# Optimization experiments

Measured on AMD Instinct MI355X. Metric: run time of the kernel, lower is better.

The kernel has to match this reference:

```python
import jax, jax.numpy as jnp
import numpy as np

B, T, D, H, S, C = 4, 2048, 1024, 16, 64, 64
LN_EPS = 1e-5
GN_EPS = 1e-5


def _layernorm(x, g, b):
    m = x.mean(-1, keepdims=True)
    v = ((x - m) ** 2).mean(-1, keepdims=True)
    return (x - m) * jax.lax.rsqrt(v + LN_EPS) * g + b


def _act_quant_ste(x):
    # clip_val computed on detached activations (matches x.detach() in torch)
    clip_val = jnp.clip(jnp.abs(jax.lax.stop_gradient(x)).mean(-1, keepdims=True), 1e-8) * 2.5
    scale = clip_val / 127.0
    xs = x / scale
    xc = jnp.clip(xs, -127.0, 127.0)
    xq = jax.lax.stop_gradient(jnp.round(xc) - xs) + xs  # straight-through round
    return xq * scale


def _weight_quant_ste(w):
    scale = jnp.clip(jnp.abs(jax.lax.stop_gradient(w)).mean(), 1e-8)
    wn = w / scale
    wc = jnp.clip(wn, -1.0, 1.0)
    wq = jax.lax.stop_gradient(jnp.round(wc) - wn) + wn  # ternary STE
    return wq * scale


def _bitlinear(x, w, g, b):
    xq = _act_quant_ste(_layernorm(x, g, b))
    wq = _weight_quant_ste(w)
    return xq @ wq.T


def _wkv_train(r, k, v, log_decay, u):
    # r,k,v: (B,H,T,S). Chunked WKV recurrence, chunk size C, state (B,H,S,S).
    dt = r.dtype
    w = jnp.exp(-jnp.exp(log_decay))            # (H,S)
    u_exp = jnp.exp(u)                          # (H,S)
    log_w = jnp.log(jnp.clip(w, 1e-38))
    t = jnp.arange(C, dtype=dt)
    # faithful to torch: diff[a,b] = clamp(t[b]-t[a],0), mask[a,b] = (t[b] >= t[a])
    diff = jnp.clip(t[None, :] - t[:, None], 0.0)
    mask = (t[None, :] >= t[:, None]).astype(dt)
    M = mask[:, :, None, None] * jnp.exp(diff[:, :, None, None] * log_w[None, None])  # (C,C,H,S)
    decay_cross = jnp.transpose(jnp.exp((t + 1.0)[:, None, None] * log_w[None]), (1, 0, 2))  # (H,C,S)
    decay_to_end = jnp.exp((C - 1.0 - t)[:, None, None] * log_w[None])  # (C,H,S)
    w_C = jnp.exp(C * log_w)  # (H,S)

    def chunk(state, rkv):
        r_c, k_c, v_c = rkv                                      # (B,H,C,S)
        kv = k_c[..., :, None] * v_c[..., None, :]               # (B,H,C,S,S)
        A = jnp.einsum('tihs,bhiso->bhtso', M, kv)               # intra-chunk
        A = A + decay_cross[None, :, :, :, None] * state[:, :, None, :, :]  # cross-chunk
        A = A + u_exp[None, :, None, :, None] * kv               # bonus term
        y_c = jnp.einsum('bhts,bhtso->bhto', r_c, A)             # (B,H,C,S)
        new_state = w_C[None, :, :, None] * state + jnp.einsum('chs,bhcso->bhso', decay_to_end, kv)
        return new_state, y_c

    chunk = jax.checkpoint(chunk)  # mirrors torch gradient checkpointing per chunk
    nC = T // C
    resh = lambda a: jnp.transpose(a.reshape(B, H, nC, C, S), (2, 0, 1, 3, 4))
    state0 = jnp.zeros((B, H, S, S), dt)
    _, ys = jax.lax.scan(chunk, state0, (resh(r), resh(k), resh(v)))  # ys: (nC,B,H,C,S)
    return jnp.transpose(ys, (1, 2, 0, 3, 4)).reshape(B, H, T, S)


def reference(x, mu_r, mu_k, mu_v, mu_g, log_decay, u, proj_w, ln_g, ln_b, gn_g, gn_b):
    # token shift: previous token, zero-padded at t=0
    xs = jnp.pad(x, ((0, 0), (1, 0), (0, 0)))[:, :-1]
    xx = xs - x

    def proj(inp, i):
        return _bitlinear(inp, proj_w[i], ln_g[i], ln_b[i])

    to_heads = lambda a: jnp.transpose(a.reshape(B, T, H, S), (0, 2, 1, 3))
    r = to_heads(proj(x + xx * mu_r, 0))
    k = to_heads(proj(x + xx * mu_k, 1))
    v = to_heads(proj(x + xx * mu_v, 2))
    g = proj(x + xx * mu_g, 3)

    y = _wkv_train(r, k, v, log_decay, u)                        # (B,H,T,S)
    y = jnp.transpose(y, (0, 2, 1, 3)).reshape(B, T, D)

    # GroupNorm(H groups over D) applied per (b,t) position
    yg = y.reshape(B, T, H, S)
    m = yg.mean(-1, keepdims=True)
    va = ((yg - m) ** 2).mean(-1, keepdims=True)
    yn = ((yg - m) * jax.lax.rsqrt(va + GN_EPS)).reshape(B, T, D)
    y = yn * gn_g + gn_b

    y = y * jax.nn.silu(g)
    return proj(y, 4)


def setup_inputs() -> dict:
    key = jax.random.key(0)
    ks = jax.random.split(key, 8)
    lid, n_layer = 16, 32
    base_decay = -4.0 + 3.0 * (lid / (n_layer - 1))
    ld = base_decay + 2.0 * (jnp.arange(S, dtype=jnp.float32) / max(S - 1, 1))
    log_decay = jnp.broadcast_to(ld, (H, S)).astype(jnp.float32)
    mu = lambda k: jax.random.uniform(k, (1, 1, D), jnp.float32, -1e-4, 1e-4)
    return {
        'x': jax.random.normal(ks[0], (B, T, D), jnp.float32),
        'mu_r': mu(ks[1]),
        'mu_k': mu(ks[2]),
        'mu_v': mu(ks[3]),
        'mu_g': mu(ks[4]),
        'log_decay': log_decay,
        'u': jax.random.normal(ks[5], (H, S), jnp.float32) * 0.02,
        'proj_w': jax.random.normal(ks[6], (5, D, D), jnp.float32) * 0.02,
        'ln_g': jnp.ones((5, D), jnp.float32),
        'ln_b': jnp.zeros((5, D), jnp.float32),
        'gn_g': jnp.ones((D,), jnp.float32),
        'gn_b': jnp.zeros((D,), jnp.float32),
    }
```

## Files before the change

### kernel.cpp

```cpp
#include <hip/hip_runtime.h>
#include <hip/hip_bf16.h>

#define BB 4
#define TT 2048
#define DD 1024
#define HH 16
#define SS 64
#define CH 64
#define NC (TT/CH)
#define M_ROWS (BB*TT)
#define COL 68

typedef __hip_bfloat16 bf16;
using int4v  = __attribute__((ext_vector_type(4))) int;
using short8 = __attribute__((ext_vector_type(8))) short;
using f32x4  = __attribute__((ext_vector_type(4))) float;

#if defined(__has_builtin)
#if __has_builtin(__builtin_amdgcn_global_load_lds)
#define HAVE_GLL 1
#endif
#if __has_builtin(__builtin_amdgcn_mfma_i32_16x16x64_i8)
#define HAVE_I8K64 1
#endif
#endif

#ifdef HAVE_GLL
static __device__ __forceinline__ void gload16(const void* g, void* l) {
  __builtin_amdgcn_global_load_lds(
      (const __attribute__((address_space(1))) void*)g,
      (__attribute__((address_space(3))) void*)l, 16, 0, 0);
}
#endif

static __device__ __forceinline__ float wave_sum(float v) {
  #pragma unroll
  for (int d = 1; d < 64; d <<= 1) v += __shfl_xor(v, d);
  return v;
}

static __device__ __forceinline__ float block_sum4(float v, float* slot, int tid) {
  float w = wave_sum(v);
  if ((tid & 63) == 0) slot[tid >> 6] = w;
  __syncthreads();
  return slot[0] + slot[1] + slot[2] + slot[3];
}

static __device__ __forceinline__ int pack4(int a, int b, int c, int d) {
  return (a & 0xff) | ((b & 0xff) << 8) | ((c & 0xff) << 16) | ((d & 0xff) << 24);
}

static __device__ __forceinline__ unsigned packsplit(float f) {
  unsigned b  = __float_as_uint(f);
  unsigned hb = b & 0xffff0000u;
  float fl = f - __uint_as_float(hb);
  unsigned lb = __float_as_uint(fl) >> 16;
  return hb | lb;
}

static __device__ __forceinline__ void unpk8(const unsigned* q, short8& h, short8& l) {
  uint4 q0 = *(const uint4*)q;
  uint4 q1 = *(const uint4*)(q + 4);
  unsigned ar[8] = {q0.x, q0.y, q0.z, q0.w, q1.x, q1.y, q1.z, q1.w};
  #pragma unroll
  for (int e = 0; e < 8; e++) {
    h[e] = (short)(ar[e] >> 16);
    l[e] = (short)(ar[e] & 0xffffu);
  }
}

__global__ __launch_bounds__(64) void k_tab(const float* __restrict__ log_decay,
                                            const float* __restrict__ u,
                                            float* __restrict__ P1t,
                                            float* __restrict__ P2t,
                                            float* __restrict__ K1Ft,
                                            float* __restrict__ K2Ft,
                                            float* __restrict__ EUt) {
  int blk = blockIdx.x;
  int h = blk >> 6, t = blk & 63;
  int s = threadIdx.x;
  float d = expf(log_decay[h * SS + s]);
  size_t idx = (size_t)blk * SS + s;
  P1t[idx]  = expf(d * (float)t);
  P2t[idx]  = expf(-d * (float)(t + 1));
  K1Ft[idx] = expf(-d * (float)t);
  K2Ft[idx] = expf(-d * (float)(63 - t));
  if (t == 0) EUt[h * SS + s] = expf(u[h * SS + s]);
}

__global__ __launch_bounds__(256) void k_wscale_part(const float* __restrict__ w,
                                                     double* __restrict__ wpart) {
  __shared__ double red[256];
  int i = blockIdx.x, b = blockIdx.y, tid = threadIdx.x;
  const float* base = w + (size_t)i * DD * DD + (size_t)b * 16384;
  double s = 0.0;
  #pragma unroll
  for (int j = 0; j < 64; j++) s += (double)fabsf(base[tid + j * 256]);
  red[tid] = s; __syncthreads();
  for (int o = 128; o > 0; o >>= 1) {
    if (tid < o) red[tid] += red[tid + o];
    __syncthreads();
  }
  if (tid == 0) wpart[i * 64 + b] = red[0];
}

__global__ __launch_bounds__(64) void k_wscale_fin(const double* __restrict__ wpart,
                                                   float* __restrict__ wscale) {
  int i = blockIdx.x;
  if (threadIdx.x == 0) {
    double s = 0.0;
    for (int b = 0; b < 64; b++) s += wpart[i * 64 + b];
    wscale[i] = fmaxf((float)(s * (1.0 / (DD * DD))), 1e-8f);
  }
}

__global__ __launch_bounds__(256) void k_wquant(const float* __restrict__ w,
                                                const float* __restrict__ wscale,
                                                char* __restrict__ wq) {
  int idx4 = (blockIdx.x * 256 + threadIdx.x) * 4;
  int i = idx4 >> 20;
  float ws = wscale[i];
  float4 w4 = *(const float4*)&w[idx4];
  float vals[4] = {w4.x, w4.y, w4.z, w4.w};
  int q[4];
  #pragma unroll
  for (int j = 0; j < 4; j++) {
    float wn = fminf(fmaxf(vals[j] / ws, -1.f), 1.f);
    q[j] = (int)rintf(wn);
  }
  *(int*)&wq[idx4] = pack4(q[0], q[1], q[2], q[3]);
}

__global__ __launch_bounds__(256) void k_prep_quant(
    const float* __restrict__ x, const float* __restrict__ mu_r,
    const float* __restrict__ mu_k, const float* __restrict__ mu_v,
    const float* __restrict__ mu_g, const float* __restrict__ ln_g,
    const float* __restrict__ ln_b, char* __restrict__ xq,
    float* __restrict__ ascale) {
  __shared__ float slots[12 * 4];
  int m = blockIdx.x, tid = threadIdx.x;
  int t = m & (TT - 1);
  const float* xr = x + (size_t)m * DD;
  int d4 = tid * 4;
  float4 xv4 = *(const float4*)&xr[d4];
  float4 xs4 = (t > 0) ? *(const float4*)&xr[d4 - DD]
                       : (float4){0.f, 0.f, 0.f, 0.f};
  float xv[4] = {xv4.x, xv4.y, xv4.z, xv4.w};
  float xs[4] = {xs4.x, xs4.y, xs4.z, xs4.w};
  const float* mus[4] = {mu_r, mu_k, mu_v, mu_g};
  #pragma unroll 1
  for (int i = 0; i < 4; i++) {
    float4 mu4 = *(const float4*)&mus[i][d4];
    float mu[4] = {mu4.x, mu4.y, mu4.z, mu4.w};
    float inp[4];
    #pragma unroll
    for (int j = 0; j < 4; j++) inp[j] = xv[j] + (xs[j] - xv[j]) * mu[j];
    float mean = block_sum4(inp[0] + inp[1] + inp[2] + inp[3],
                            &slots[(i * 3 + 0) * 4], tid) * (1.f / DD);
    float var = 0.f;
    #pragma unroll
    for (int j = 0; j < 4; j++) { float dv = inp[j] - mean; var += dv * dv; }
    var = block_sum4(var, &slots[(i * 3 + 1) * 4], tid) * (1.f / DD);
    float rstd = 1.f / sqrtf(var + 1e-5f);
    float4 lg4 = *(const float4*)&ln_g[i * DD + d4];
    float4 lb4 = *(const float4*)&ln_b[i * DD + d4];
    float lg[4] = {lg4.x, lg4.y, lg4.z, lg4.w};
    float lb[4] = {lb4.x, lb4.y, lb4.z, lb4.w};
    float ln[4]; float aabs = 0.f;
    #pragma unroll
    for (int j = 0; j < 4; j++) {
      ln[j] = (inp[j] - mean) * rstd * lg[j] + lb[j];
      aabs += fabsf(ln[j]);
    }
    float meanabs = block_sum4(aabs, &slots[(i * 3 + 2) * 4], tid) * (1.f / DD);
    float scale = fmaxf(meanabs, 1e-8f) * 2.5f * (1.f / 127.f);
    int q[4];
    #pragma unroll
    for (int j = 0; j < 4; j++)
      q[j] = (int)rintf(fminf(fmaxf(ln[j] / scale, -127.f), 127.f));
    *(int*)&xq[((size_t)i * M_ROWS + m) * DD + d4] = pack4(q[0], q[1], q[2], q[3]);
    if (tid == 0) ascale[i * M_ROWS + m] = scale;
  }
}

__global__ __launch_bounds__(512) void k_gemm(
    const char* __restrict__ Axq, const char* __restrict__ Wq,
    const float* __restrict__ ascale, const float* __restrict__ wscale,
    int projbase, float* __restrict__ outF) {
  __shared__ __align__(16) char As[3][256 * 64];
  __shared__ __align__(16) char Bs[3][256 * 64];
  int tid = threadIdx.x;
  int wvid = tid >> 6, lane = tid & 63;
  int wm = wvid >> 2, wn = wvid & 3;
  int m0 = blockIdx.x * 256, n0 = blockIdx.y * 256;
  int z = blockIdx.z;
  int proj = projbase + z;
  const char* Ap = Axq + ((size_t)z * M_ROWS + m0) * DD;
  const char* Wp = Wq + ((size_t)proj * DD + n0) * DD;
  int4v acc[8][4];
  #pragma unroll
  for (int i = 0; i < 8; i++)
    #pragma unroll
    for (int j = 0; j < 4; j++) acc[i][j] = (int4v){0, 0, 0, 0};

  int frow = lane & 15, fslot = lane >> 4;
  int srow_lo = tid >> 2;
  int sslot0  = tid & 3;

  auto stage_pass = [&](int k0, int q, char* Ad, char* Bd) {
    int rr = ((q & 1) << 7) + srow_lo;
    int sl = sslot0 ^ ((rr >> 1) & 3);
    if (q < 2) {
#ifdef HAVE_GLL
      gload16(&Ap[(size_t)rr * DD + k0 + sl * 16], &Ad[(q & 1) * 8192 + tid * 16]);
#else
      *(uint4*)&Ad[(q & 1) * 8192 + tid * 16] =
          *(const uint4*)&Ap[(size_t)rr * DD + k0 + sl * 16];
#endif
    } else {
#ifdef HAVE_GLL
      gload16(&Wp[(size_t)rr * DD + k0 + sl * 16], &Bd[(q & 1) * 8192 + tid * 16]);
#else
      *(uint4*)&Bd[(q & 1) * 8192 + tid * 16] =
          *(const uint4*)&Wp[(size_t)rr * DD + k0 + sl * 16];
#endif
    }
  };

  #pragma unroll
  for (int q = 0; q < 4; q++) stage_pass(0, q, As[0], Bs[0]);
  #pragma unroll
  for (int q = 0; q < 4; q++) stage_pass(64, q, As[1], Bs[1]);
#ifdef HAVE_GLL
  asm volatile("s_waitcnt vmcnt(4)" ::: "memory");
  __builtin_amdgcn_s_barrier();
#else
  __syncthreads();
#endif

  for (int kt = 0; kt < 16; ++kt) {
    const char* Abuf = As[kt % 3];
    const char* Bbuf = Bs[kt % 3];
    char* Anx = As[(kt + 2) % 3];
    char* Bnx = Bs[(kt + 2) % 3];
    int k0n = (kt + 2) * 64;
    bool do_stage = (kt + 2) < 16;
    int4v bfr[4];
    #pragma unroll
    for (int j = 0; j < 4; j++) {
      int r = 64 * wn + 16 * j + frow;
      bfr[j] = *(const int4v*)&Bbuf[r * 64 + (fslot ^ ((r >> 1) & 3)) * 16];
    }
    #pragma unroll
    for (int p = 0; p < 4; p++) {
      if (do_stage) stage_pass(k0n, p, Anx, Bnx);
      int4v af[2];
      #pragma unroll
      for (int e = 0; e < 2; e++) {
        int r = 128 * wm + 16 * (2 * p + e) + frow;
        af[e] = *(const int4v*)&Abuf[r * 64 + (fslot ^ ((r >> 1) & 3)) * 16];
      }
      __builtin_amdgcn_s_setprio(1);
#ifdef HAVE_I8K64
      #pragma unroll
      for (int e = 0; e < 2; e++)
        #pragma unroll
        for (int j = 0; j < 4; j++)
          acc[2 * p + e][j] =
              __builtin_amdgcn_mfma_i32_16x16x64_i8(af[e], bfr[j], acc[2 * p + e][j], 0, 0, 0);
#else
      #pragma unroll
      for (int e = 0; e < 2; e++)
        #pragma unroll
        for (int j = 0; j < 4; j++)
          #pragma unroll
          for (int hh2 = 0; hh2 < 2; hh2++) {
            long a8, b8;
            memcpy(&a8, ((const char*)&af[e]) + hh2 * 8, 8);
            memcpy(&b8, ((const char*)&bfr[j]) + hh2 * 8, 8);
            acc[2 * p + e][j] =
                __builtin_amdgcn_mfma_i32_16x16x32_i8(a8, b8, acc[2 * p + e][j], 0, 0, 0);
          }
#endif
      __builtin_amdgcn_s_setprio(0);
    }
    if (kt < 15) {
#ifdef HAVE_GLL
      if (kt + 2 < 16) asm volatile("s_waitcnt vmcnt(4)" ::: "memory");
      else             asm volatile("s_waitcnt vmcnt(0)" ::: "memory");
      __builtin_amdgcn_s_barrier();
#else
      __syncthreads();
#endif
    }
  }

  const float* asc = ascale + (size_t)z * M_ROWS + m0;
  float wsc = wscale[proj];
  int col = lane & 15, rg = lane >> 4;
  #pragma unroll
  for (int i = 0; i < 8; i++) {
    #pragma unroll
    for (int r = 0; r < 4; r++) {
      int mm = 128 * wm + 16 * i + rg * 4 + r;
      float s = asc[mm] * wsc;
      #pragma unroll
      for (int j = 0; j < 4; j++) {
        int nn = 64 * wn + 16 * j + col;
        outF[((size_t)z * M_ROWS + m0 + mm) * DD + (n0 + nn)] = (float)acc[i][j][r] * s;
      }
    }
  }
}

__global__ __launch_bounds__(256) void k_inj_mm(const float* __restrict__ rkvg,
                                                const float* __restrict__ K2Ft,
                                                float* __restrict__ states) {
#if defined(__HIP_DEVICE_COMPILE__)
  __shared__ __align__(16) unsigned k2t[64 * COL];
  __shared__ __align__(16) unsigned vtsh[64 * COL];
  int blk = blockIdx.x, tid = threadIdx.x;
  int n = blk & (NC - 1), h = (blk >> 5) & (HH - 1), b = blk >> 9;
  size_t rowbase = ((size_t)b * TT + n * CH) * DD + h * SS;
  const float* Kp = rkvg + (size_t)1 * M_ROWS * DD + rowbase;
  const float* Vp = rkvg + (size_t)2 * M_ROWS * DD + rowbase;
  const float* K2h = K2Ft + (size_t)h * SS * SS;

  int s_me = tid & 63, c0 = tid >> 6;
  #pragma unroll 4
  for (int j = 0; j < 16; j++) {
    int c = c0 + 4 * j;
    float kv = Kp[(size_t)c * DD + s_me];
    float vv = Vp[(size_t)c * DD + s_me];
    k2t[s_me * COL + c] = packsplit(kv * K2h[(size_t)c * SS + s_me]);
    vtsh[s_me * COL + c] = packsplit(vv);
  }
  __syncthreads();

  int wid = tid >> 6, lane = tid & 63;
  int s_row = wid * 16 + (lane & 15);
  int koff = (lane >> 4) * 8;
  short8 ah[2], al[2];
  #pragma unroll
  for (int kh = 0; kh < 2; kh++)
    unpk8(&k2t[s_row * COL + kh * 32 + koff], ah[kh], al[kh]);

  float* st = states + (size_t)blk * SS * SS;
  #pragma unroll 1
  for (int ot = 0; ot < 4; ot++) {
    int o_row = ot * 16 + (lane & 15);
    f32x4 acc = {0.f, 0.f, 0.f, 0.f};
    #pragma unroll
    for (int kh = 0; kh < 2; kh++) {
      short8 vh, vl;
      unpk8(&vtsh[o_row * COL + kh * 32 + koff], vh, vl);
      acc = __builtin_amdgcn_mfma_f32_16x16x32_bf16(ah[kh], vh, acc, 0, 0, 0);
      acc = __builtin_amdgcn_mfma_f32_16x16x32_bf16(ah[kh], vl, acc, 0, 0, 0);
      acc = __builtin_amdgcn_mfma_f32_16x16x32_bf16(al[kh], vh, acc, 0, 0, 0);
    }
    #pragma unroll
    for (int rr = 0; rr < 4; rr++) {
      int s = wid * 16 + (lane >> 4) * 4 + rr;
      int o = ot * 16 + (lane & 15);
      st[(size_t)s * SS + o] = acc[rr];
    }
  }
#endif
}

__global__ __launch_bounds__(256) void k_scan(const float* __restrict__ log_decay,
                                              float* __restrict__ states) {
  int blk = blockIdx.x;
  int bh = blk >> 4, sb = blk & 15;
  int h = bh & (HH - 1);
  int tid = threadIdx.x;
  int js = tid >> 6, o = tid & 63;
  int s = sb * 4 + js;
  float wC = expf(-64.f * expf(log_decay[h * SS + s]));
  float* base = states + (size_t)bh * NC * SS * SS + (size_t)s * SS + o;
  float inj[NC];
  #pragma unroll
  for (int n = 0; n < NC; n++) inj[n] = base[(size_t)n * SS * SS];
  float cur = 0.f;
  #pragma unroll
  for (int n = 0; n < NC; n++) {
    base[(size_t)n * SS * SS] = cur;
    cur = fmaf(wC, cur, inj[n]);
  }
}

__global__ __launch_bounds__(256) void k_wkv_mm(const float* __restrict__ rkvg,
                                                const float* __restrict__ states,
                                                const float* __restrict__ P1t,
                                                const float* __restrict__ P2t,
                                                const float* __restrict__ K1Ft,
                                                const float* __restrict__ EUt,
                                                float* __restrict__ Y) {
#if defined(__HIP_DEVICE_COMPILE__)
  __shared__ __align__(16) float    rsh[64 * COL];
  __shared__ __align__(16) unsigned k1sh[64 * COL];
  __shared__ __align__(16) unsigned vtsh[64 * COL];
  unsigned* Pls = (unsigned*)rsh;

  int blk = blockIdx.x, tid = threadIdx.x;
  int n = blk & (NC - 1), h = (blk >> 5) & (HH - 1), b = blk >> 9;
  size_t rowbase = ((size_t)b * TT + n * CH) * DD + h * SS;
  const float* Rp = rkvg + rowbase;
  const float* Kp = rkvg + (size_t)1 * M_ROWS * DD + rowbase;
  const float* Vp = rkvg + (size_t)2 * M_ROWS * DD + rowbase;
  const float* stp = states + (size_t)blk * SS * SS;
  const float* P1h = P1t + (size_t)h * SS * SS;
  const float* P2h = P2t + (size_t)h * SS * SS;
  const float* K1h = K1Ft + (size_t)h * SS * SS;

  int s_me = tid & 63, c0 = tid >> 6;
  float stv[16];
  #pragma unroll 4
  for (int j = 0; j < 16; j++) {
    int c = c0 + 4 * j;
    float rv = Rp[(size_t)c * DD + s_me];
    float kv = Kp[(size_t)c * DD + s_me];
    float vv = Vp[(size_t)c * DD + s_me];
    stv[j] = stp[(size_t)c * SS + s_me];
    rsh[c * COL + s_me] = rv;
    k1sh[c * COL + s_me] = packsplit(kv * K1h[(size_t)c * SS + s_me]);
    vtsh[s_me * COL + c] = packsplit(vv);
  }
  __syncthreads();

  int wid = tid >> 6, lane = tid & 63;
  int t_row = wid * 16 + (lane & 15);
  int koff = (lane >> 4) * 8;

  short8 a1h[2], a1l[2], a2h[2], a2l[2];
  #pragma unroll
  for (int kh = 0; kh < 2; kh++) {
    int sb0 = kh * 32 + koff;
    size_t tb = (size_t)t_row * SS + sb0;
    float4 p1a = *(const float4*)&P1h[tb], p1b = *(const float4*)&P1h[tb + 4];
    float4 p2a = *(const float4*)&P2h[tb], p2b = *(const float4*)&P2h[tb + 4];
    float4 rva = *(const float4*)&rsh[t_row * COL + sb0];
    float4 rvb = *(const float4*)&rsh[t_row * COL + sb0 + 4];
    float p1[8] = {p1a.x, p1a.y, p1a.z, p1a.w, p1b.x, p1b.y, p1b.z, p1b.w};
    float p2[8] = {p2a.x, p2a.y, p2a.z, p2a.w, p2b.x, p2b.y, p2b.z, p2b.w};
    float rv[8] = {rva.x, rva.y, rva.z, rva.w, rvb.x, rvb.y, rvb.z, rvb.w};
    #pragma unroll
    for (int e = 0; e < 8; e++) {
      unsigned u1 = packsplit(rv[e] * p1[e]);
      unsigned u2 = packsplit(rv[e] * p2[e]);
      a1h[kh][e] = (short)(u1 >> 16); a1l[kh][e] = (short)(u1 & 0xffffu);
      a2h[kh][e] = (short)(u2 >> 16); a2l[kh][e] = (short)(u2 & 0xffffu);
    }
  }

  #pragma unroll 1
  for (int it = 0; it < 4; it++) {
    int i_row = it * 16 + (lane & 15);
    f32x4 acc = {0.f, 0.f, 0.f, 0.f};
    f32x4 accu = {0.f, 0.f, 0.f, 0.f};
    bool anyKeep = (it >= wid);
    bool diag = (it == wid);
    if (anyKeep) {
      #pragma unroll
      for (int kh = 0; kh < 2; kh++) {
        const unsigned* q = &k1sh[i_row * COL + kh * 32 + koff];
        uint4 q0 = *(const uint4*)q;
        uint4 q1 = *(const uint4*)(q + 4);
        unsigned ar[8] = {q0.x, q0.y, q0.z, q0.w, q1.x, q1.y, q1.z, q1.w};
        short8 bh, bl;
        #pragma unroll
        for (int e = 0; e < 8; e++) {
          bh[e] = (short)(ar[e] >> 16);
          bl[e] = (short)(ar[e] & 0xffffu);
        }
        acc = __builtin_amdgcn_mfma_f32_16x16x32_bf16(a1h[kh], bh, acc, 0, 0, 0);
        acc = __builtin_amdgcn_mfma_f32_16x16x32_bf16(a1h[kh], bl, acc, 0, 0, 0);
        acc = __builtin_amdgcn_mfma_f32_16x16x32_bf16(a1l[kh], bh, acc, 0, 0, 0);
        if (diag) {
          int sb0 = kh * 32 + koff;
          float4 eua = *(const float4*)&EUt[h * SS + sb0];
          float4 eub = *(const float4*)&EUt[h * SS + sb0 + 4];
          float eu[8] = {eua.x, eua.y, eua.z, eua.w, eub.x, eub.y, eub.z, eub.w};
          short8 bhu, blu;
          #pragma unroll
          for (int e = 0; e < 8; e++) {
            float k1f = __uint_as_float(ar[e] & 0xffff0000u)
                      + __uint_as_float((ar[e] & 0xffffu) << 16);
            unsigned pu = packsplit(k1f * eu[e]);
            bhu[e] = (short)(pu >> 16); blu[e] = (short)(pu & 0xffffu);
          }
          accu = __builtin_amdgcn_mfma_f32_16x16x32_bf16(a1h[kh], bhu, accu, 0, 0, 0);
          accu = __builtin_amdgcn_mfma_f32_16x16x32_bf16(a1h[kh], blu, accu, 0, 0, 0);
          accu = __builtin_amdgcn_mfma_f32_16x16x32_bf16(a1l[kh], bhu, accu, 0, 0, 0);
        }
      }
    }
    #pragma unroll
    for (int rr = 0; rr < 4; rr++) {
      int trow = wid * 16 + (lane >> 4) * 4 + rr;
      int icol = it * 16 + (lane & 15);
      float p = acc[rr];
      p = (icol < trow) ? 0.f : p;
      if (icol == trow) p += accu[rr];
      Pls[trow * COL + icol] = packsplit(p);
    }
  }
  __syncthreads();

  unsigned* stsh = k1sh;
  #pragma unroll
  for (int j = 0; j < 16; j++) {
    int c = c0 + 4 * j;
    stsh[s_me * COL + c] = packsplit(stv[j]);
  }
  __syncthreads();

  float* Yb = Y + ((size_t)b * TT + n * CH) * DD + h * SS;
  #pragma unroll 1
  for (int ot = 0; ot < 4; ot++) {
    int o_row = ot * 16 + (lane & 15);
    f32x4 acc = {0.f, 0.f, 0.f, 0.f};
    #pragma unroll
    for (int kh = 0; kh < 2; kh++) {
      short8 ph, pl, vh, vl, sh2, sl2;
      unpk8(&Pls[t_row * COL + kh * 32 + koff], ph, pl);
      unpk8(&vtsh[o_row * COL + kh * 32 + koff], vh, vl);
      acc = __builtin_amdgcn_mfma_f32_16x16x32_bf16(ph, vh, acc, 0, 0, 0);
      acc = __builtin_amdgcn_mfma_f32_16x16x32_bf16(ph, vl, acc, 0, 0, 0);
      acc = __builtin_amdgcn_mfma_f32_16x16x32_bf16(pl, vh, acc, 0, 0, 0);
      unpk8(&stsh[o_row * COL + kh * 32 + koff], sh2, sl2);
      acc = __builtin_amdgcn_mfma_f32_16x16x32_bf16(a2h[kh], sh2, acc, 0, 0, 0);
      acc = __builtin_amdgcn_mfma_f32_16x16x32_bf16(a2h[kh], sl2, acc, 0, 0, 0);
      acc = __builtin_amdgcn_mfma_f32_16x16x32_bf16(a2l[kh], sh2, acc, 0, 0, 0);
    }
    #pragma unroll
    for (int rr = 0; rr < 4; rr++) {
      int trow = wid * 16 + (lane >> 4) * 4 + rr;
      int oc = ot * 16 + (lane & 15);
      Yb[(size_t)trow * DD + oc] = acc[rr];
    }
  }
#endif
}

__global__ __launch_bounds__(256) void k_post(const float* __restrict__ Y,
                                              const float* __restrict__ G,
                                              const float* __restrict__ gn_g,
                                              const float* __restrict__ gn_b,
                                              const float* __restrict__ lg,
                                              const float* __restrict__ lb,
                                              char* __restrict__ xq4,
                                              float* __restrict__ ascale4) {
  __shared__ float slots[3 * 4];
  __shared__ float gmean[HH], grstd[HH];
  int m = blockIdx.x, tid = threadIdx.x;
  int d4 = tid * 4;
  float4 y4v = *(const float4*)&Y[(size_t)m * DD + d4];
  float4 g4v = *(const float4*)&G[(size_t)m * DD + d4];
  float y4[4] = {y4v.x, y4v.y, y4v.z, y4v.w};
  float g4[4] = {g4v.x, g4v.y, g4v.z, g4v.w};
  {
    float s = y4[0] + y4[1] + y4[2] + y4[3];
    s += __shfl_xor(s, 1); s += __shfl_xor(s, 2);
    s += __shfl_xor(s, 4); s += __shfl_xor(s, 8);
    float mn = s * (1.f / SS);
    float v2 = 0.f;
    #pragma unroll
    for (int q = 0; q < 4; q++) { float dv = y4[q] - mn; v2 += dv * dv; }
    v2 += __shfl_xor(v2, 1); v2 += __shfl_xor(v2, 2);
    v2 += __shfl_xor(v2, 4); v2 += __shfl_xor(v2, 8);
    if ((tid & 15) == 0) {
      gmean[tid >> 4] = mn;
      grstd[tid >> 4] = 1.f / sqrtf(v2 * (1.f / SS) + 1e-5f);
    }
  }
  __syncthreads();
  int hh = tid >> 4;
  float4 gg4 = *(const float4*)&gn_g[d4];
  float4 gb4 = *(const float4*)&gn_b[d4];
  float gg[4] = {gg4.x, gg4.y, gg4.z, gg4.w};
  float gb[4] = {gb4.x, gb4.y, gb4.z, gb4.w};
  float z[4];
  #pragma unroll
  for (int j = 0; j < 4; j++) {
    float yn = (y4[j] - gmean[hh]) * grstd[hh] * gg[j] + gb[j];
    float gv = g4[j];
    z[j] = yn * (gv / (1.f + expf(-gv)));
  }
  float mean = block_sum4(z[0] + z[1] + z[2] + z[3], &slots[0], tid) * (1.f / DD);
  float var = 0.f;
  #pragma unroll
  for (int j = 0; j < 4; j++) { float dv = z[j] - mean; var += dv * dv; }
  var = block_sum4(var, &slots[4], tid) * (1.f / DD);
  float rstd = 1.f / sqrtf(var + 1e-5f);
  float4 lg4 = *(const float4*)&lg[d4];
  float4 lb4 = *(const float4*)&lb[d4];
  float lgv[4] = {lg4.x, lg4.y, lg4.z, lg4.w};
  float lbv[4] = {lb4.x, lb4.y, lb4.z, lb4.w};
  float ln[4]; float aabs = 0.f;
  #pragma unroll
  for (int j = 0; j < 4; j++) {
    ln[j] = (z[j] - mean) * rstd * lgv[j] + lbv[j];
    aabs += fabsf(ln[j]);
  }
  float meanabs = block_sum4(aabs, &slots[8], tid) * (1.f / DD);
  float scale = fmaxf(meanabs, 1e-8f) * 2.5f * (1.f / 127.f);
  int q[4];
  #pragma unroll
  for (int j = 0; j < 4; j++)
    q[j] = (int)rintf(fminf(fmaxf(ln[j] / scale, -127.f), 127.f));
  *(int*)&xq4[(size_t)m * DD + d4] = pack4(q[0], q[1], q[2], q[3]);
  if (tid == 0) ascale4[m] = scale;
}

extern "C" void kernel_launch(void* const* d_in, const int* in_sizes, int n_in,
                              void* d_out, int out_size, void* d_ws, size_t ws_size,
                              hipStream_t stream) {
  const float* x         = (const float*)d_in[0];
  const float* mu_r      = (const float*)d_in[1];
  const float* mu_k      = (const float*)d_in[2];
  const float* mu_v      = (const float*)d_in[3];
  const float* mu_g      = (const float*)d_in[4];
  const float* log_decay = (const float*)d_in[5];
  const float* u         = (const float*)d_in[6];
  const float* proj_w    = (const float*)d_in[7];
  const float* ln_g      = (const float*)d_in[8];
  const float* ln_b      = (const float*)d_in[9];
  const float* gn_g      = (const float*)d_in[10];
  const float* gn_b      = (const float*)d_in[11];
  float* out = (float*)d_out;

  char* p = (char*)d_ws;
  float*  wscale = (float*)p;  p += 256;
  double* wpart  = (double*)p; p += 4096;
  char*   wq     = (char*)p;   p += (size_t)5 * DD * DD;
  float*  ascale = (float*)p;  p += (size_t)5 * M_ROWS * 4;
  char*   U      = p;          p += (size_t)40 * 1024 * 1024;
  char*   xq     = U;
  float*  Y      = (float*)U;
  char*   xq4    = U + (size_t)M_ROWS * DD * 4;
  float*  rkvg   = (float*)p;  p += (size_t)4 * M_ROWS * DD * 4;
  float*  states = (float*)p;  p += (size_t)BB * HH * NC * SS * SS * 4;
  float*  P1t    = (float*)p;  p += (size_t)HH * SS * SS * 4;
  float*  P2t    = (float*)p;  p += (size_t)HH * SS * SS * 4;
  float*  K1Ft   = (float*)p;  p += (size_t)HH * SS * SS * 4;
  float*  K2Ft   = (float*)p;  p += (size_t)HH * SS * SS * 4;
  float*  EUt    = (float*)p;  p += (size_t)HH * SS * 4;

  hipLaunchKernelGGL(k_tab, dim3(HH * SS), dim3(64), 0, stream,
                     log_decay, u, P1t, P2t, K1Ft, K2Ft, EUt);
  hipLaunchKernelGGL(k_wscale_part, dim3(5, 64), dim3(256), 0, stream, proj_w, wpart);
  hipLaunchKernelGGL(k_wscale_fin, dim3(5), dim3(64), 0, stream, wpart, wscale);
  hipLaunchKernelGGL(k_wquant, dim3((5 * DD * DD) / 1024), dim3(256), 0, stream,
                     proj_w, wscale, wq);
  hipLaunchKernelGGL(k_prep_quant, dim3(M_ROWS), dim3(256), 0, stream,
                     x, mu_r, mu_k, mu_v, mu_g, ln_g, ln_b, xq, ascale);
  hipLaunchKernelGGL(k_gemm, dim3(M_ROWS / 256, DD / 256, 4), dim3(512), 0,
                     stream, xq, wq, ascale, wscale, 0, rkvg);
  hipLaunchKernelGGL(k_inj_mm, dim3(BB * HH * NC), dim3(256), 0, stream,
                     rkvg, K2Ft, states);
  hipLaunchKernelGGL(k_scan, dim3(BB * HH * 16), dim3(256), 0, stream,
                     log_decay, states);
  hipLaunchKernelGGL(k_wkv_mm, dim3(BB * HH * NC), dim3(256), 0, stream,
                     rkvg, states, P1t, P2t, K1Ft, EUt, Y);
  hipLaunchKernelGGL(k_post, dim3(M_ROWS), dim3(256), 0, stream,
                     Y, rkvg + (size_t)3 * M_ROWS * DD, gn_g, gn_b,
                     ln_g + 4 * DD, ln_b + 4 * DD,
                     xq4, ascale + 4 * M_ROWS);
  hipLaunchKernelGGL(k_gemm, dim3(M_ROWS / 256, DD / 256, 1), dim3(512), 0,
                     stream, xq4, wq,
                     ascale + 4 * M_ROWS, wscale, 4, out);
}
```

Before: 333.8 us.

## Use per-wave row reductions in prep and smaller-tile GEMM for output projection

The activation prep kernel now processes one row per wavefront, using wave-level reductions instead of LDS block reductions and barriers. The final output projection switches to a new 128x128-tile int8 MFMA GEMM with double buffering, launching more blocks so the single-projection GEMM fills more compute units. The smaller tile lowers data reuse per block and adds a second GEMM kernel to maintain.

```diff
diff --git a/kernel.cpp b/kernel.cpp
--- a/kernel.cpp
+++ b/kernel.cpp
@@ -137,49 +137,73 @@
     const float* __restrict__ mu_g, const float* __restrict__ ln_g,
     const float* __restrict__ ln_b, char* __restrict__ xq,
     float* __restrict__ ascale) {
-  __shared__ float slots[12 * 4];
-  int m = blockIdx.x, tid = threadIdx.x;
+  int tid = threadIdx.x;
+  int wid = tid >> 6, lane = tid & 63;
+  int m = blockIdx.x * 4 + wid;
   int t = m & (TT - 1);
   const float* xr = x + (size_t)m * DD;
-  int d4 = tid * 4;
-  float4 xv4 = *(const float4*)&xr[d4];
-  float4 xs4 = (t > 0) ? *(const float4*)&xr[d4 - DD]
+  float xv[16], xs[16];
+  #pragma unroll
+  for (int i = 0; i < 4; i++) {
+    int d0 = lane * 4 + 256 * i;
+    float4 v = *(const float4*)&xr[d0];
+    xv[4 * i + 0] = v.x; xv[4 * i + 1] = v.y;
+    xv[4 * i + 2] = v.z; xv[4 * i + 3] = v.w;
+    float4 s = (t > 0) ? *(const float4*)&xr[d0 - DD]
                        : (float4){0.f, 0.f, 0.f, 0.f};
-  float xv[4] = {xv4.x, xv4.y, xv4.z, xv4.w};
-  float xs[4] = {xs4.x, xs4.y, xs4.z, xs4.w};
+    xs[4 * i + 0] = s.x; xs[4 * i + 1] = s.y;
+    xs[4 * i + 2] = s.z; xs[4 * i + 3] = s.w;
+  }
   const float* mus[4] = {mu_r, mu_k, mu_v, mu_g};
   #pragma unroll 1
-  for (int i = 0; i < 4; i++) {
-    float4 mu4 = *(const float4*)&mus[i][d4];
-    float mu[4] = {mu4.x, mu4.y, mu4.z, mu4.w};
-    float inp[4];
-    #pragma unroll
-    for (int j = 0; j < 4; j++) inp[j] = xv[j] + (xs[j] - xv[j]) * mu[j];
-    float mean = block_sum4(inp[0] + inp[1] + inp[2] + inp[3],
-                            &slots[(i * 3 + 0) * 4], tid) * (1.f / DD);
+  for (int p = 0; p < 4; p++) {
+    float inp[16];
+    float sum = 0.f;
+    #pragma unroll
+    for (int i = 0; i < 4; i++) {
+      int d0 = lane * 4 + 256 * i;
+      float4 mu4 = *(const float4*)&mus[p][d0];
+      float mu[4] = {mu4.x, mu4.y, mu4.z, mu4.w};
+      #pragma unroll
+      for (int j = 0; j < 4; j++) {
+        int e = 4 * i + j;
+        inp[e] = xv[e] + (xs[e] - xv[e]) * mu[j];
+        sum += inp[e];
+      }
+    }
+    float mean = wave_sum(sum) * (1.f / DD);
     float var = 0.f;
     #pragma unroll
-    for (int j = 0; j < 4; j++) { float dv = inp[j] - mean; var += dv * dv; }
-    var = block_sum4(var, &slots[(i * 3 + 1) * 4], tid) * (1.f / DD);
+    for (int e = 0; e < 16; e++) { float dv = inp[e] - mean; var += dv * dv; }
+    var = wave_sum(var) * (1.f / DD);
     float rstd = 1.f / sqrtf(var + 1e-5f);
-    float4 lg4 = *(const float4*)&ln_g[i * DD + d4];
-    float4 lb4 = *(const float4*)&ln_b[i * DD + d4];
-    float lg[4] = {lg4.x, lg4.y, lg4.z, lg4.w};
-    float lb[4] = {lb4.x, lb4.y, lb4.z, lb4.w};
-    float ln[4]; float aabs = 0.f;
-    #pragma unroll
-    for (int j = 0; j < 4; j++) {
-      ln[j] = (inp[j] - mean) * rstd * lg[j] + lb[j];
-      aabs += fabsf(ln[j]);
-    }
-    float meanabs = block_sum4(aabs, &slots[(i * 3 + 2) * 4], tid) * (1.f / DD);
+    float ln[16]; float aabs = 0.f;
+    #pragma unroll
+    for (int i = 0; i < 4; i++) {
+      int d0 = lane * 4 + 256 * i;
+      float4 lg4 = *(const float4*)&ln_g[p * DD + d0];
+      float4 lb4 = *(const float4*)&ln_b[p * DD + d0];
+      float lg[4] = {lg4.x, lg4.y, lg4.z, lg4.w};
+      float lb[4] = {lb4.x, lb4.y, lb4.z, lb4.w};
+      #pragma unroll
+      for (int j = 0; j < 4; j++) {
+        int e = 4 * i + j;
+        ln[e] = (inp[e] - mean) * rstd * lg[j] + lb[j];
+        aabs += fabsf(ln[e]);
+      }
+    }
+    float meanabs = wave_sum(aabs) * (1.f / DD);
     float scale = fmaxf(meanabs, 1e-8f) * 2.5f * (1.f / 127.f);
-    int q[4];
-    #pragma unroll
-    for (int j = 0; j < 4; j++)
-      q[j] = (int)rintf(fminf(fmaxf(ln[j] / scale, -127.f), 127.f));
-    *(int*)&xq[((size_t)i * M_ROWS + m) * DD + d4] = pack4(q[0], q[1], q[2], q[3]);
-    if (tid == 0) ascale[i * M_ROWS + m] = scale;
+    char* xo = xq + ((size_t)p * M_ROWS + m) * DD;
+    #pragma unroll
+    for (int i = 0; i < 4; i++) {
+      int q[4];
+      #pragma unroll
+      for (int j = 0; j < 4; j++)
+        q[j] = (int)rintf(fminf(fmaxf(ln[4 * i + j] / scale, -127.f), 127.f));
+      *(int*)&xo[lane * 4 + 256 * i] = pack4(q[0], q[1], q[2], q[3]);
+    }
+    if (lane == 0) ascale[p * M_ROWS + m] = scale;
   }
 }
 
@@ -303,6 +327,107 @@
     #pragma unroll
     for (int r = 0; r < 4; r++) {
       int mm = 128 * wm + 16 * i + rg * 4 + r;
+      float s = asc[mm] * wsc;
+      #pragma unroll
+      for (int j = 0; j < 4; j++) {
+        int nn = 64 * wn + 16 * j + col;
+        outF[((size_t)z * M_ROWS + m0 + mm) * DD + (n0 + nn)] = (float)acc[i][j][r] * s;
+      }
+    }
+  }
+}
+
+__global__ __launch_bounds__(256) void k_gemm128(
+    const char* __restrict__ Axq, const char* __restrict__ Wq,
+    const float* __restrict__ ascale, const float* __restrict__ wscale,
+    int projbase, float* __restrict__ outF) {
+  __shared__ __align__(16) char As[2][128 * 64];
+  __shared__ __align__(16) char Bs[2][128 * 64];
+  int tid = threadIdx.x;
+  int wvid = tid >> 6, lane = tid & 63;
+  int wm = wvid >> 1, wn = wvid & 1;
+  int m0 = blockIdx.x * 128, n0 = blockIdx.y * 128;
+  int z = blockIdx.z;
+  int proj = projbase + z;
+  const char* Ap = Axq + ((size_t)z * M_ROWS + m0) * DD;
+  const char* Wp = Wq + ((size_t)proj * DD + n0) * DD;
+  int4v acc[4][4];
+  #pragma unroll
+  for (int i = 0; i < 4; i++)
+    #pragma unroll
+    for (int j = 0; j < 4; j++) acc[i][j] = (int4v){0, 0, 0, 0};
+  int row = tid >> 2, col16 = (tid & 3) * 16;
+  int frow = lane & 15, fq16 = (lane >> 4) * 16;
+
+  auto stage = [&](int k0, int buf) {
+    #pragma unroll
+    for (int q = 0; q < 2; q++) {
+#ifdef HAVE_GLL
+      gload16(&Ap[(size_t)(q * 64 + row) * DD + k0 + col16],
+              &As[buf][q * 4096 + tid * 16]);
+      gload16(&Wp[(size_t)(q * 64 + row) * DD + k0 + col16],
+              &Bs[buf][q * 4096 + tid * 16]);
+#else
+      *(uint4*)&As[buf][(q * 64 + row) * 64 + col16] =
+          *(const uint4*)&Ap[(size_t)(q * 64 + row) * DD + k0 + col16];
+      *(uint4*)&Bs[buf][(q * 64 + row) * 64 + col16] =
+          *(const uint4*)&Wp[(size_t)(q * 64 + row) * DD + k0 + col16];
+#endif
+    }
+  };
+
+  stage(0, 0);
+  __syncthreads();
+  int cur = 0;
+  for (int k0 = 0; k0 < DD; k0 += 64) {
+    if (k0 + 64 < DD) stage(k0 + 64, cur ^ 1);
+#ifdef HAVE_I8K64
+    int4v af[4], bfr[4];
+    #pragma unroll
+    for (int i = 0; i < 4; i++)
+      af[i] = *(const int4v*)&As[cur][(64 * wm + 16 * i + frow) * 64 + fq16];
+    #pragma unroll
+    for (int j = 0; j < 4; j++)
+      bfr[j] = *(const int4v*)&Bs[cur][(64 * wn + 16 * j + frow) * 64 + fq16];
+    #pragma unroll
+    for (int i = 0; i < 4; i++)
+      #pragma unroll
+      for (int j = 0; j < 4; j++)
+        acc[i][j] = __builtin_amdgcn_mfma_i32_16x16x64_i8(af[i], bfr[j], acc[i][j], 0, 0, 0);
+#else
+    int fq8 = (lane >> 4) * 8;
+    long afl[4][2], bfl[4][2];
+    #pragma unroll
+    for (int i = 0; i < 4; i++)
+      #pragma unroll
+      for (int h = 0; h < 2; h++)
+        afl[i][h] = *(const long*)&As[cur][(64 * wm + 16 * i + frow) * 64 + h * 32 + fq8];
+    #pragma unroll
+    for (int j = 0; j < 4; j++)
+      #pragma unroll
+      for (int h = 0; h < 2; h++)
+        bfl[j][h] = *(const long*)&Bs[cur][(64 * wn + 16 * j + frow) * 64 + h * 32 + fq8];
+    #pragma unroll
+    for (int i = 0; i < 4; i++)
+      #pragma unroll
+      for (int j = 0; j < 4; j++)
+        #pragma unroll
+        for (int h = 0; h < 2; h++)
+          acc[i][j] = __builtin_amdgcn_mfma_i32_16x16x32_i8(afl[i][h], bfl[j][h], acc[i][j], 0, 0, 0);
+#endif
+    if (k0 + 64 < DD) {
+      __syncthreads();
+      cur ^= 1;
+    }
+  }
+  const float* asc = ascale + (size_t)z * M_ROWS + m0;
+  float wsc = wscale[proj];
+  int col = lane & 15, rg = lane >> 4;
+  #pragma unroll
+  for (int i = 0; i < 4; i++) {
+    #pragma unroll
+    for (int r = 0; r < 4; r++) {
+      int mm = 64 * wm + 16 * i + rg * 4 + r;
       float s = asc[mm] * wsc;
       #pragma unroll
       for (int j = 0; j < 4; j++) {
@@ -653,7 +778,7 @@
   hipLaunchKernelGGL(k_wscale_fin, dim3(5), dim3(64), 0, stream, wpart, wscale);
   hipLaunchKernelGGL(k_wquant, dim3((5 * DD * DD) / 1024), dim3(256), 0, stream,
                      proj_w, wscale, wq);
-  hipLaunchKernelGGL(k_prep_quant, dim3(M_ROWS), dim3(256), 0, stream,
+  hipLaunchKernelGGL(k_prep_quant, dim3(M_ROWS / 4), dim3(256), 0, stream,
                      x, mu_r, mu_k, mu_v, mu_g, ln_g, ln_b, xq, ascale);
   hipLaunchKernelGGL(k_gemm, dim3(M_ROWS / 256, DD / 256, 4), dim3(512), 0,
                      stream, xq, wq, ascale, wscale, 0, rkvg);
@@ -667,7 +792,7 @@
                      Y, rkvg + (size_t)3 * M_ROWS * DD, gn_g, gn_b,
                      ln_g + 4 * DD, ln_b + 4 * DD,
                      xq4, ascale + 4 * M_ROWS);
-  hipLaunchKernelGGL(k_gemm, dim3(M_ROWS / 256, DD / 256, 1), dim3(512), 0,
+  hipLaunchKernelGGL(k_gemm128, dim3(M_ROWS / 128, DD / 128, 1), dim3(256), 0,
                      stream, xq4, wq,
                      ascale + 4 * M_ROWS, wscale, 4, out);
 }
```

Measured after the change: 308.1 us. -7.7%, faster.
